# Performance work log

Hardware: AMD Instinct MI355X
Metric: run time of the kernel (lower is better)

Reference implementation:

```python
import jax, jax.numpy as jnp
import numpy as np

B, DIM, EMBDIM = 32, 512, 512
MEMSIZE, MEMSEQ = 32, 64
VOCAB = 50257


def setup_inputs() -> dict:
    key = jax.random.key(0)
    ks = jax.random.split(key, 10)
    inp = {
        'enc': jax.random.normal(ks[0], (B, DIM), jnp.float32),
        'encsumm': jax.random.normal(ks[1], (B, DIM), jnp.float32),
        'embsumm': jax.random.normal(ks[2], (B, EMBDIM), jnp.float32),
        'memencs': jax.random.normal(ks[3], (B, MEMSIZE, MEMSEQ, DIM), jnp.float32),
        'memencsumm': jax.random.normal(ks[4], (B, MEMSIZE, MEMSEQ, DIM), jnp.float32),
        'memembsumm': jax.random.normal(ks[5], (B, MEMSIZE, MEMSEQ, EMBDIM), jnp.float32),
        'memmask': jnp.ones((B, MEMSIZE, MEMSEQ), jnp.float32),
        'memids': jax.random.randint(ks[6], (B, MEMSIZE, MEMSEQ), 0, VOCAB, jnp.int64 if jax.config.jax_enable_x64 else jnp.int32),
        'W_out': jax.random.normal(ks[7], (VOCAB, 2 * DIM), jnp.float32) * 0.02,
        'b_out': jnp.zeros((VOCAB,), jnp.float32),
        'W_mix': jax.random.normal(ks[8], (2, 2 * DIM), jnp.float32) * 0.02,
        'b_mix': jnp.zeros((2,), jnp.float32),
        'unktok_mask': jnp.ones((VOCAB,), jnp.float32),  # no unktoks
    }
    return inp


def reference(enc, encsumm, embsumm, memencs, memencsumm, memembsumm, memmask,
              memids, W_out, b_out, W_mix, b_mix, unktok_mask):
    # copy branch: attention over flattened memory, scatter-add into vocab
    query = jnp.concatenate([embsumm, jnp.zeros_like(encsumm), enc], axis=-1)        # (B, 2*dim+embdim)
    keys = jnp.concatenate([memembsumm, jnp.zeros_like(memencsumm), memencs], axis=-1)  # (B, M, Z, 2*dim+embdim)
    w = jnp.einsum('bd,bmzd->bmz', query, keys) + jnp.log(memmask)
    b = w.shape[0]
    w = w.reshape(b, -1)                                    # (B, M*Z)
    alphas = jax.nn.softmax(w, axis=-1)
    mem_flat = memencs.reshape(b, -1, memencs.shape[-1])    # (B, M*Z, dim)
    mem_enc_summ = jnp.einsum('bm,bmd->bd', alphas, mem_flat)
    toks = memids.reshape(b, -1)                            # (B, M*Z)
    rows = jnp.arange(b)[:, None]
    vocsize = W_out.shape[0]
    probs_mem = jnp.zeros((b, vocsize), alphas.dtype).at[rows, toks].add(alphas)
    # generation branch
    h = jnp.concatenate([encsumm, enc], axis=-1)            # (B, 2*dim)
    logits_gen = h @ W_out.T + b_out + jnp.log(unktok_mask)[None, :]
    probs_gen = jax.nn.softmax(logits_gen, axis=-1)
    # mixer combine
    mix = jax.nn.softmax(h @ W_mix.T + b_mix, axis=-1)      # (B, 2)
    probs = mix[:, 0:1] * probs_gen + mix[:, 1:2] * probs_mem
    # original stack/gather trick: selects probs where nonzero, zeros where zero -> identity
    probs = jnp.where(probs != 0, probs, jnp.zeros_like(probs))
    return probs, mem_enc_summ
```

## Files before the change

kernel.cpp:

```cpp
#include <hip/hip_runtime.h>
#include <hip/hip_bf16.h>

#define NB   32
#define DIMK 512
#define MM   32
#define ZZ   64
#define MZV  2048
#define VOC  50257
#define NK4  1571

typedef __attribute__((ext_vector_type(8))) short  short8;
typedef __attribute__((ext_vector_type(4))) float  f32x4;
typedef __attribute__((ext_vector_type(8))) unsigned short ushort8;

#define WS_W      0
#define WS_PVEC   (WS_W + NB*MZV)
#define WS_LSTAT  (WS_PVEC + NB*MM*DIMK)
#define WS_GSTATW (WS_LSTAT + NB*MM*2)
#define WS_MIX    (WS_GSTATW + NB*2)
#define WS_GPART  (WS_MIX + NB*2)

__device__ __forceinline__ ushort8 cvt8(float4 a, float4 b) {
    union { ushort8 u; __hip_bfloat162 h[4]; } r;
    r.h[0] = __float22bfloat162_rn(make_float2(a.x, a.y));
    r.h[1] = __float22bfloat162_rn(make_float2(a.z, a.w));
    r.h[2] = __float22bfloat162_rn(make_float2(b.x, b.y));
    r.h[3] = __float22bfloat162_rn(make_float2(b.z, b.w));
    return r.u;
}

typedef const __attribute__((address_space(1))) void* gas_t;
typedef __attribute__((address_space(3))) void*       las_t;
__device__ __forceinline__ void gload16(const void* g, void* l) {
    __builtin_amdgcn_global_load_lds((gas_t)g, (las_t)l, 16, 0, 0);
}

__global__ __launch_bounds__(256, 6) void k14_fused(
    const float* __restrict__ enc, const float* __restrict__ embsumm,
    const float* __restrict__ encsumm,
    const float* __restrict__ memencs, const float* __restrict__ memembsumm,
    const float* __restrict__ memmask,
    const float* __restrict__ W_out, const float* __restrict__ b_out,
    const float* __restrict__ unk, float* __restrict__ out,
    float* __restrict__ ws)
{
    __shared__ __align__(16) union {
        struct { float sacc[4][DIMK]; float sst[4][2]; } s1;
        struct { float w[2][2048]; unsigned short a[2][2048]; } s4;
    } smem;

    int bid = blockIdx.x;
    int tid = threadIdx.x, wid = tid >> 6, lane = tid & 63;
    bool isK1; int sub;
    if (bid < 2048) { isK1 = ((bid & 1) == 0); sub = bid >> 1; }
    else            { isK1 = false;            sub = bid - 1024; }

    if (isK1) {
        int b = sub >> 5, m = sub & 31;
        int c0 = lane * 4, c1 = c0 + 256;
        const float* encb = enc + b * DIMK;
        const float* embb = embsumm + b * DIMK;
        float4 qe0 = *(const float4*)(encb + c0);
        float4 qe1 = *(const float4*)(encb + c1);
        float4 qm0 = *(const float4*)(embb + c0);
        float4 qm1 = *(const float4*)(embb + c1);
        const float* meb = memencs    + (long)(b*MM + m) * ZZ * DIMK;
        const float* mmb = memembsumm + (long)(b*MM + m) * ZZ * DIMK;
        const float* mkb = memmask    + (long)(b*MM + m) * ZZ;
        float* w_ws = ws + WS_W + b*MZV + m*ZZ;

        float lmax = -3.0e38f, lsum = 0.f;
        float4 a0 = make_float4(0.f,0.f,0.f,0.f), a1 = make_float4(0.f,0.f,0.f,0.f);

        for (int z = wid; z < ZZ; z += 4) {
            const float* mer = meb + z*DIMK;
            const float* mmr = mmb + z*DIMK;
            float4 e0 = *(const float4*)(mer + c0);
            float4 e1 = *(const float4*)(mer + c1);
            float4 s0 = *(const float4*)(mmr + c0);
            float4 s1 = *(const float4*)(mmr + c1);
            float d = e0.x*qe0.x + e0.y*qe0.y + e0.z*qe0.z + e0.w*qe0.w
                    + e1.x*qe1.x + e1.y*qe1.y + e1.z*qe1.z + e1.w*qe1.w
                    + s0.x*qm0.x + s0.y*qm0.y + s0.z*qm0.z + s0.w*qm0.w
                    + s1.x*qm1.x + s1.y*qm1.y + s1.z*qm1.z + s1.w*qm1.w;
            #pragma unroll
            for (int off = 32; off; off >>= 1) d += __shfl_xor(d, off);
            d += logf(mkb[z]);
            if (lane == 0) w_ws[z] = d;
            float nm = fmaxf(lmax, d);
            float sc = __expf(lmax - nm);
            float e  = __expf(d - nm);
            lsum = lsum * sc + e;
            a0.x = a0.x*sc + e*e0.x; a0.y = a0.y*sc + e*e0.y;
            a0.z = a0.z*sc + e*e0.z; a0.w = a0.w*sc + e*e0.w;
            a1.x = a1.x*sc + e*e1.x; a1.y = a1.y*sc + e*e1.y;
            a1.z = a1.z*sc + e*e1.z; a1.w = a1.w*sc + e*e1.w;
            lmax = nm;
        }

        *(float4*)&smem.s1.sacc[wid][c0] = a0;
        *(float4*)&smem.s1.sacc[wid][c1] = a1;
        if (lane == 0) { smem.s1.sst[wid][0] = lmax; smem.s1.sst[wid][1] = lsum; }
        __syncthreads();
        float bm = fmaxf(fmaxf(smem.s1.sst[0][0], smem.s1.sst[1][0]),
                         fmaxf(smem.s1.sst[2][0], smem.s1.sst[3][0]));
        float sc0 = __expf(smem.s1.sst[0][0]-bm), sc1 = __expf(smem.s1.sst[1][0]-bm);
        float sc2 = __expf(smem.s1.sst[2][0]-bm), sc3 = __expf(smem.s1.sst[3][0]-bm);
        float bs = smem.s1.sst[0][1]*sc0 + smem.s1.sst[1][1]*sc1
                 + smem.s1.sst[2][1]*sc2 + smem.s1.sst[3][1]*sc3;
        int d0 = tid * 2;
        float2 v0 = *(float2*)&smem.s1.sacc[0][d0];
        float2 v1 = *(float2*)&smem.s1.sacc[1][d0];
        float2 v2 = *(float2*)&smem.s1.sacc[2][d0];
        float2 v3 = *(float2*)&smem.s1.sacc[3][d0];
        float p0 = v0.x*sc0 + v1.x*sc1 + v2.x*sc2 + v3.x*sc3;
        float p1 = v0.y*sc0 + v1.y*sc1 + v2.y*sc2 + v3.y*sc3;
        float* pv = ws + WS_PVEC + (long)(b*MM+m)*DIMK + d0;
        pv[0] = p0; pv[1] = p1;
        if (tid == 0) { float* ls = ws + WS_LSTAT + (b*MM+m)*2; ls[0] = bm; ls[1] = bs; }
    } else {
        int wv = wid >> 1, wb = wid & 1;
        int vt = sub * 32;

        int idx0 = (wid*2 + 0)*64 + lane;
        int idx1 = (wid*2 + 1)*64 + lane;
        int wr0 = idx0 >> 4, wq0 = idx0 & 15;
        int wr1 = idx1 >> 4, wq1 = idx1 & 15;
        const float* wsrc0 = W_out + (long)min(vt + wr0, VOC-1)*1024 + ((wq0 ^ (wr0 & 7))*4);
        const float* wsrc1 = W_out + (long)min(vt + wr1, VOC-1)*1024 + ((wq1 ^ (wr1 & 7))*4);
        int ar = tid >> 3, ag = tid & 7;
        const float* hs0 = encsumm + ar*DIMK + ag*8;
        const float* hs1 = enc     + ar*DIMK + ag*8;
        int awpos = ar*64 + ((ag ^ (ar & 7))*8);

#define ISSUE_W(c, buf) do {                                          \
            gload16(wsrc0 + (c)*64, &smem.s4.w[buf][idx0*4]);         \
            gload16(wsrc1 + (c)*64, &smem.s4.w[buf][idx1*4]); } while (0)
#define LOADA(c) do { const float* hp = ((c) < 8 ? hs0 + (c)*64 : hs1 + ((c)-8)*64); \
            af0 = *(const float4*)(hp); af1 = *(const float4*)(hp + 4); } while (0)
#define WRITEA(buf) do { *(ushort8*)&smem.s4.a[buf][awpos] = cvt8(af0, af1); } while (0)

        int lg = lane >> 4, ln = lane & 15;
        int vrow = wv*16 + ln;
        int ab   = wb*16 + ln;
        f32x4 acc = {0.f, 0.f, 0.f, 0.f};
        float4 af0, af1;

        LOADA(0); WRITEA(0);
        LOADA(1); WRITEA(1);
        LOADA(2);
        ISSUE_W(0, 0);
        ISSUE_W(1, 1);
        __syncthreads();

        for (int c = 0; c < 16; ++c) {
            int buf = c & 1;
            #pragma unroll
            for (int s = 0; s < 2; ++s) {
                int q = s*8 + lg*2;
                float4 b0 = *(const float4*)&smem.s4.w[buf][vrow*64 + ((q    ) ^ (vrow & 7))*4];
                float4 b1 = *(const float4*)&smem.s4.w[buf][vrow*64 + ((q + 1) ^ (vrow & 7))*4];
                int g = s*4 + lg;
                short8 afrag = *(const short8*)&smem.s4.a[buf][ab*64 + ((g ^ (ab & 7)))*8];
                ushort8 bu = cvt8(b0, b1);
                short8 bfrag = *(short8*)&bu;
                acc = __builtin_amdgcn_mfma_f32_16x16x32_bf16(afrag, bfrag, acc, 0, 0, 0);
            }
            __syncthreads();
            if (c + 2 < 16) {
                WRITEA(buf);
                ISSUE_W(c + 2, buf);
                if (c + 3 < 16) LOADA(c + 3);
            }
        }
#undef ISSUE_W
#undef LOADA
#undef WRITEA

        int v = vt + vrow;
        if (v < VOC) {
            float bias = b_out[v] + logf(unk[v]);
            #pragma unroll
            for (int rr = 0; rr < 4; ++rr) {
                int m = wb*16 + lg*4 + rr;
                out[(long)m*VOC + v] = acc[rr] + bias;
            }
        }
    }
}

__global__ __launch_bounds__(256) void k2k5(
    const float* __restrict__ encsumm, const float* __restrict__ enc,
    const float* __restrict__ W_mix, const float* __restrict__ b_mix,
    float* __restrict__ out, float* __restrict__ ws)
{
    int bid = blockIdx.x, tid = threadIdx.x;
    if (bid < 32) {
        int b = bid;
        const float* ls = ws + WS_LSTAT + b*MM*2;
        float gm = -3.0e38f;
        #pragma unroll
        for (int m = 0; m < MM; m++) gm = fmaxf(gm, ls[m*2]);
        float gs = 0.f;
        #pragma unroll
        for (int m = 0; m < MM; m++) gs += ls[m*2+1] * __expf(ls[m*2] - gm);
        if (tid == 0) { ws[WS_GSTATW + b*2] = gm; ws[WS_GSTATW + b*2 + 1] = gs; }
        float inv = 1.0f / gs;
        int d0 = tid * 2;
        float p0 = 0.f, p1 = 0.f;
        for (int m = 0; m < MM; m++) {
            float sc = __expf(ls[m*2] - gm);
            const float* pv = ws + WS_PVEC + (long)(b*MM+m)*DIMK + d0;
            p0 += pv[0]*sc; p1 += pv[1]*sc;
        }
        out[(long)NB*VOC + b*DIMK + d0]     = p0 * inv;
        out[(long)NB*VOC + b*DIMK + d0 + 1] = p1 * inv;

        if (tid < 64) {
            int l = tid;
            float m0 = 0.f, m1 = 0.f;
            #pragma unroll
            for (int p = 0; p < 4; p++) {
                int cc = l*4 + p*256;
                float4 h4 = (cc < 512) ? *(const float4*)(encsumm + b*DIMK + cc)
                                       : *(const float4*)(enc + b*DIMK + cc - 512);
                float4 w0 = *(const float4*)(W_mix + cc);
                float4 w1 = *(const float4*)(W_mix + 1024 + cc);
                m0 += h4.x*w0.x + h4.y*w0.y + h4.z*w0.z + h4.w*w0.w;
                m1 += h4.x*w1.x + h4.y*w1.y + h4.z*w1.z + h4.w*w1.w;
            }
            #pragma unroll
            for (int off = 32; off; off >>= 1) { m0 += __shfl_xor(m0, off); m1 += __shfl_xor(m1, off); }
            if (l == 0) {
                m0 += b_mix[0]; m1 += b_mix[1];
                float mx = fmaxf(m0, m1);
                float e0 = __expf(m0-mx), e1 = __expf(m1-mx);
                float s = e0 + e1;
                ws[WS_MIX + b*2] = e0/s; ws[WS_MIX + b*2 + 1] = e1/s;
            }
        }
    } else {
        int sub = bid - 32;
        int chunk = sub & 31, b = sub >> 5;
        const float* logits = out;
        const int CH = (VOC + 31) / 32;
        int v0 = chunk * CH;
        int v1 = min(VOC, v0 + CH);
        float m = -3.0e38f, s = 0.f;
        for (int v = v0 + tid; v < v1; v += 256) {
            float x = logits[(long)b*VOC + v];
            float nm = fmaxf(m, x);
            s = s*__expf(m - nm) + __expf(x - nm);
            m = nm;
        }
        #pragma unroll
        for (int off = 32; off; off >>= 1) {
            float om = __shfl_xor(m, off), os = __shfl_xor(s, off);
            float nm = fmaxf(m, om);
            s = s*__expf(m - nm) + os*__expf(om - nm);
            m = nm;
        }
        __shared__ float sm[4], ssum[4];
        int wid = tid >> 6, lane = tid & 63;
        if (lane == 0) { sm[wid] = m; ssum[wid] = s; }
        __syncthreads();
        if (tid == 0) {
            float gm = fmaxf(fmaxf(sm[0], sm[1]), fmaxf(sm[2], sm[3]));
            float gs = ssum[0]*__expf(sm[0]-gm) + ssum[1]*__expf(sm[1]-gm)
                     + ssum[2]*__expf(sm[2]-gm) + ssum[3]*__expf(sm[3]-gm);
            ws[WS_GPART + (b*32 + chunk)*2]     = gm;
            ws[WS_GPART + (b*32 + chunk)*2 + 1] = gs;
        }
    }
}

__global__ __launch_bounds__(256) void k6_final(float* __restrict__ probs, const float* __restrict__ ws)
{
    int v = blockIdx.x*256 + threadIdx.x;
    int b = blockIdx.y;
    float gm = -3.0e38f;
    #pragma unroll
    for (int i = 0; i < 32; ++i) gm = fmaxf(gm, ws[WS_GPART + (b*32+i)*2]);
    float gs = 0.f;
    #pragma unroll
    for (int i = 0; i < 32; ++i)
        gs += ws[WS_GPART + (b*32+i)*2 + 1] * __expf(ws[WS_GPART + (b*32+i)*2] - gm);
    if (v >= VOC) return;
    float mix0 = ws[WS_MIX + b*2];
    long idx = (long)b*VOC + v;
    probs[idx] = mix0 * __expf(probs[idx] - gm) / gs;
}

__global__ __launch_bounds__(256) void k7_scatter(const int* __restrict__ memids,
                                                  const float* __restrict__ ws,
                                                  float* __restrict__ probs)
{
    int idx = blockIdx.x*256 + threadIdx.x;
    int b = idx >> 11, mz = idx & 2047;
    float gm = ws[WS_GSTATW + b*2], gs = ws[WS_GSTATW + b*2 + 1];
    float mix1 = ws[WS_MIX + b*2 + 1];
    float alpha = __expf(ws[WS_W + b*MZV + mz] - gm) / gs;
    int tok = memids[b*MZV + mz];
    atomicAdd(&probs[(long)b*VOC + tok], mix1 * alpha);
}

extern "C" void kernel_launch(void* const* d_in, const int* in_sizes, int n_in,
                              void* d_out, int out_size, void* d_ws, size_t ws_size,
                              hipStream_t stream)
{
    const float* enc        = (const float*)d_in[0];
    const float* encsumm    = (const float*)d_in[1];
    const float* embsumm    = (const float*)d_in[2];
    const float* memencs    = (const float*)d_in[3];
    const float* memembsumm = (const float*)d_in[5];
    const float* memmask    = (const float*)d_in[6];
    const int*   memids     = (const int*)d_in[7];
    const float* W_out      = (const float*)d_in[8];
    const float* b_out      = (const float*)d_in[9];
    const float* W_mix      = (const float*)d_in[10];
    const float* b_mix      = (const float*)d_in[11];
    const float* unk        = (const float*)d_in[12];
    float* out = (float*)d_out;
    float* ws  = (float*)d_ws;

    hipLaunchKernelGGL(k14_fused, dim3(1024 + NK4), dim3(256), 0, stream,
                       enc, embsumm, encsumm, memencs, memembsumm, memmask,
                       W_out, b_out, unk, out, ws);
    hipLaunchKernelGGL(k2k5, dim3(32 + 1024), dim3(256), 0, stream,
                       encsumm, enc, W_mix, b_mix, out, ws);
    hipLaunchKernelGGL(k6_final, dim3((VOC + 255)/256, NB), dim3(256), 0, stream, out, ws);
    hipLaunchKernelGGL(k7_scatter, dim3(NB*MZV/256), dim3(256), 0, stream, memids, ws, out);
}
```

Measured before the change: 129.4 us.

## Deepen GEMV tile pipeline to 4 buffers with async LDS loads for both operands

Replaces the double-buffered 64-wide K chunks with a 4-stage ring of 32-wide chunks, loading both W_out and the activation tile directly into LDS via global_load_lds and using explicit vmcnt waits plus a single barrier per step. Activations are now converted to bf16 in registers at use time rather than staged as bf16. This aims to keep more memory requests in flight for the bandwidth-bound W_out stream. The trade-offs are twice as many iterations, each with a barrier, redundant fp32 activation loads and conversions, and a lower occupancy hint (5 instead of 6).

```diff
diff --git a/kernel.cpp b/kernel.cpp
--- a/kernel.cpp
+++ b/kernel.cpp
@@ -35,7 +35,7 @@
     __builtin_amdgcn_global_load_lds((gas_t)g, (las_t)l, 16, 0, 0);
 }
 
-__global__ __launch_bounds__(256, 6) void k14_fused(
+__global__ __launch_bounds__(256, 5) void k14_fused(
     const float* __restrict__ enc, const float* __restrict__ embsumm,
     const float* __restrict__ encsumm,
     const float* __restrict__ memencs, const float* __restrict__ memembsumm,
@@ -46,7 +46,7 @@
 {
     __shared__ __align__(16) union {
         struct { float sacc[4][DIMK]; float sst[4][2]; } s1;
-        struct { float w[2][2048]; unsigned short a[2][2048]; } s4;
+        struct { float w[4][1024]; float a[4][1024]; } s4;
     } smem;
 
     int bid = blockIdx.x;
@@ -122,60 +122,45 @@
         int wv = wid >> 1, wb = wid & 1;
         int vt = sub * 32;
 
-        int idx0 = (wid*2 + 0)*64 + lane;
-        int idx1 = (wid*2 + 1)*64 + lane;
-        int wr0 = idx0 >> 4, wq0 = idx0 & 15;
-        int wr1 = idx1 >> 4, wq1 = idx1 & 15;
-        const float* wsrc0 = W_out + (long)min(vt + wr0, VOC-1)*1024 + ((wq0 ^ (wr0 & 7))*4);
-        const float* wsrc1 = W_out + (long)min(vt + wr1, VOC-1)*1024 + ((wq1 ^ (wr1 & 7))*4);
-        int ar = tid >> 3, ag = tid & 7;
-        const float* hs0 = encsumm + ar*DIMK + ag*8;
-        const float* hs1 = enc     + ar*DIMK + ag*8;
-        int awpos = ar*64 + ((ag ^ (ar & 7))*8);
-
-#define ISSUE_W(c, buf) do {                                          \
-            gload16(wsrc0 + (c)*64, &smem.s4.w[buf][idx0*4]);         \
-            gload16(wsrc1 + (c)*64, &smem.s4.w[buf][idx1*4]); } while (0)
-#define LOADA(c) do { const float* hp = ((c) < 8 ? hs0 + (c)*64 : hs1 + ((c)-8)*64); \
-            af0 = *(const float4*)(hp); af1 = *(const float4*)(hp + 4); } while (0)
-#define WRITEA(buf) do { *(ushort8*)&smem.s4.a[buf][awpos] = cvt8(af0, af1); } while (0)
+        int srow = tid >> 3, sq = tid & 7;
+        int sqs = sq ^ (srow & 7);
+        const float* wbase = W_out + (long)min(vt + srow, VOC-1)*1024 + sqs*4;
+        int aoff = srow*DIMK + sqs*4;
+        int ldst = tid * 4;
+
+#define ISSUE(ch, bf) do {                                                   \
+            gload16(wbase + (ch)*32, &smem.s4.w[bf][ldst]);                  \
+            const float* asp = (((ch) < 16) ? encsumm : enc) + aoff + ((ch)&15)*32; \
+            gload16(asp, &smem.s4.a[bf][ldst]); } while (0)
 
         int lg = lane >> 4, ln = lane & 15;
         int vrow = wv*16 + ln;
         int ab   = wb*16 + ln;
+        int wq0 = (vrow*8 + ((lg*2)     ^ (vrow & 7))) * 4;
+        int wq1 = (vrow*8 + ((lg*2 + 1) ^ (vrow & 7))) * 4;
+        int aq0 = (ab*8   + ((lg*2)     ^ (ab & 7)))   * 4;
+        int aq1 = (ab*8   + ((lg*2 + 1) ^ (ab & 7)))   * 4;
         f32x4 acc = {0.f, 0.f, 0.f, 0.f};
-        float4 af0, af1;
-
-        LOADA(0); WRITEA(0);
-        LOADA(1); WRITEA(1);
-        LOADA(2);
-        ISSUE_W(0, 0);
-        ISSUE_W(1, 1);
-        __syncthreads();
-
-        for (int c = 0; c < 16; ++c) {
-            int buf = c & 1;
-            #pragma unroll
-            for (int s = 0; s < 2; ++s) {
-                int q = s*8 + lg*2;
-                float4 b0 = *(const float4*)&smem.s4.w[buf][vrow*64 + ((q    ) ^ (vrow & 7))*4];
-                float4 b1 = *(const float4*)&smem.s4.w[buf][vrow*64 + ((q + 1) ^ (vrow & 7))*4];
-                int g = s*4 + lg;
-                short8 afrag = *(const short8*)&smem.s4.a[buf][ab*64 + ((g ^ (ab & 7)))*8];
-                ushort8 bu = cvt8(b0, b1);
-                short8 bfrag = *(short8*)&bu;
-                acc = __builtin_amdgcn_mfma_f32_16x16x32_bf16(afrag, bfrag, acc, 0, 0, 0);
-            }
-            __syncthreads();
-            if (c + 2 < 16) {
-                WRITEA(buf);
-                ISSUE_W(c + 2, buf);
-                if (c + 3 < 16) LOADA(c + 3);
-            }
-        }
-#undef ISSUE_W
-#undef LOADA
-#undef WRITEA
+
+        ISSUE(0, 0); ISSUE(1, 1); ISSUE(2, 2);
+
+        for (int c = 0; c < 32; ++c) {
+            if (c <= 29)      asm volatile("s_waitcnt vmcnt(4)" ::: "memory");
+            else if (c == 30) asm volatile("s_waitcnt vmcnt(2)" ::: "memory");
+            else              asm volatile("s_waitcnt vmcnt(0)" ::: "memory");
+            __builtin_amdgcn_s_barrier();
+            if (c + 3 < 32) ISSUE(c + 3, (c + 3) & 3);
+            int bf = c & 3;
+            float4 b0 = *(const float4*)&smem.s4.w[bf][wq0];
+            float4 b1 = *(const float4*)&smem.s4.w[bf][wq1];
+            float4 a0 = *(const float4*)&smem.s4.a[bf][aq0];
+            float4 a1 = *(const float4*)&smem.s4.a[bf][aq1];
+            ushort8 bu = cvt8(b0, b1);
+            ushort8 au = cvt8(a0, a1);
+            acc = __builtin_amdgcn_mfma_f32_16x16x32_bf16(*(short8*)&au, *(short8*)&bu,
+                                                          acc, 0, 0, 0);
+        }
+#undef ISSUE
 
         int v = vt + vrow;
         if (v < VOC) {
```

Result: slower. 132.2 us (+2.2%).
